# Performance work log

Measured on AMD Instinct MI355X. Metric: run time of the kernel, lower is better.

The kernel has to match this reference:

```python
import jax, jax.numpy as jnp
import numpy as np
from jax import lax

TOPK = 32
EPS = 1e-5


def setup_inputs() -> dict:
    key = jax.random.key(0)
    k1, k2, k3, k4 = jax.random.split(key, 4)
    t, b, dim = 1024, 2, 1024
    heads, num_keys, dim_head = 4, 512, 256
    dim_query = heads * dim_head  # 1024
    x = jax.random.normal(k1, (t, b, dim), dtype=jnp.float32)
    # nn.Linear default init ~ U(-1/sqrt(in), 1/sqrt(in)); scaled normal is fine as data
    Wq = jax.random.normal(k2, (dim, dim_query), dtype=jnp.float32) * (1.0 / np.sqrt(dim))
    gamma = jnp.ones((dim_query,), dtype=jnp.float32)
    beta = jnp.zeros((dim_query,), dtype=jnp.float32)
    # init_weights: keys std = 1/last_dim; values std = 1/sqrt(dim)
    keys = jax.random.normal(k3, (heads, num_keys, 2, dim_head // 2), dtype=jnp.float32) * (1.0 / (dim_head // 2))
    values = jax.random.normal(k4, (num_keys ** 2, dim), dtype=jnp.float32) * (1.0 / np.sqrt(dim))
    return {"x": x, "Wq": Wq, "gamma": gamma, "beta": beta, "keys": keys, "values": values}


def reference(x, Wq, gamma, beta, keys, values):
    t, b, e = x.shape
    h, n, _, dh2 = keys.shape  # heads, num_keys, 2, dim_head//2
    k = TOPK

    # queries = LayerNorm(x @ Wq)
    q = jnp.einsum('tbe,ef->tbf', x, Wq)  # (t, b, h*2*dh2)
    mu = jnp.mean(q, axis=-1, keepdims=True)
    var = jnp.var(q, axis=-1, keepdims=True)
    q = (q - mu) / jnp.sqrt(var + EPS) * gamma + beta

    # chunk into two halves of the query dim, each reshaped to (h, dh2)
    q = jnp.stack(jnp.split(q, 2, axis=-1)).reshape(2, t, b, h, dh2)  # (p=2, t, b, h, d)

    # scores against product keys
    dots = jnp.einsum('ptbhd,hnpd->tbhpn', q, keys)  # (t, b, h, 2, n)
    scores, indices = lax.top_k(dots, k)             # (t, b, h, 2, k)

    s1, s2 = scores[..., 0, :], scores[..., 1, :]
    i1, i2 = indices[..., 0, :], indices[..., 1, :]

    # cartesian product of the two top-k sets
    all_scores = (s1[..., :, None] + s2[..., None, :]).reshape(t, b, h, k * k)
    all_indices = (i1[..., :, None] * n + i2[..., None, :]).reshape(t, b, h, k * k)

    final_scores, final_idx = lax.top_k(all_scores, k)              # (t, b, h, k)
    value_indices = jnp.take_along_axis(all_indices, final_idx, axis=-1)
    attn = jax.nn.softmax(final_scores, axis=-1)

    value_indices = value_indices.reshape(t * b, h * k)
    attn = attn.reshape(t * b, h * k)

    # EmbeddingBag(mode='sum') with per_sample_weights
    gathered = values[value_indices]                 # (t*b, h*k, e)
    out = jnp.einsum('nk,nke->ne', attn, gathered)
    return out.reshape(t, b, e)
```

## Files before the change

### kernel.cpp

```cpp
#include <hip/hip_runtime.h>
#include <math.h>

#define NTOK 2048
#define DIM  1024
#define NHEAD 4
#define NKEY 512
#define DH   128
#define TK   32

typedef __attribute__((ext_vector_type(8))) short bf16x8;
typedef __attribute__((ext_vector_type(4))) float f32x4;

__device__ __forceinline__ unsigned short f2bf(float f) {
    unsigned int u = __float_as_uint(f);
    u += 0x7fff + ((u >> 16) & 1);
    return (unsigned short)(u >> 16);
}
__device__ __forceinline__ float bf2f(unsigned short h) {
    return __uint_as_float(((unsigned int)h) << 16);
}
__device__ __forceinline__ void split3(float f, unsigned short& h, unsigned short& m, unsigned short& l) {
    h = f2bf(f);
    float r1 = f - bf2f(h);
    m = f2bf(r1);
    l = f2bf(r1 - bf2f(m));
}
__device__ __forceinline__ void gll16(const void* g, void* l) {
    __builtin_amdgcn_global_load_lds((const __attribute__((address_space(1))) unsigned int*)g,
                                     (__attribute__((address_space(3))) unsigned int*)l, 16, 0, 0);
}

__global__ __launch_bounds__(256) void k_prep(const float* __restrict__ x,
                                              const float* __restrict__ Wq,
                                              const float* __restrict__ keys,
                                              unsigned short* __restrict__ X1,
                                              unsigned short* __restrict__ X2,
                                              unsigned short* __restrict__ X3,
                                              unsigned short* __restrict__ W1,
                                              unsigned short* __restrict__ W2,
                                              unsigned short* __restrict__ W3,
                                              unsigned short* __restrict__ K1,
                                              unsigned short* __restrict__ K2,
                                              unsigned short* __restrict__ K3) {
    __shared__ float f[64][33];
    const int b = blockIdx.x, tid = threadIdx.x;
    if (b < 2048) {
        int i = b * 256 + tid;
        float4 v = ((const float4*)x)[i];
        ushort4 hh, mm, ll;
        split3(v.x, hh.x, mm.x, ll.x); split3(v.y, hh.y, mm.y, ll.y);
        split3(v.z, hh.z, mm.z, ll.z); split3(v.w, hh.w, mm.w, ll.w);
        ((ushort4*)X1)[i] = hh; ((ushort4*)X2)[i] = mm; ((ushort4*)X3)[i] = ll;
    } else if (b < 2560) {
        const int ff = b - 2048;
        const int kt = (ff & 15) * 64, nt = (ff >> 4) * 32;
#pragma unroll
        for (int i = 0; i < 8; ++i) {
            int idx = tid + i * 256;
            int nl = idx & 31, kl = idx >> 5;
            f[kl][nl] = Wq[(size_t)(kt + kl) * DIM + nt + nl];
        }
        __syncthreads();
#pragma unroll
        for (int i = 0; i < 2; ++i) {
            int idx = tid + i * 256;
            int k4 = (idx & 15) * 4, nl = idx >> 4;
            ushort4 hh, mm, ll;
            split3(f[k4 + 0][nl], hh.x, mm.x, ll.x);
            split3(f[k4 + 1][nl], hh.y, mm.y, ll.y);
            split3(f[k4 + 2][nl], hh.z, mm.z, ll.z);
            split3(f[k4 + 3][nl], hh.w, mm.w, ll.w);
            *(ushort4*)(W1 + (size_t)(nt + nl) * DIM + kt + k4) = hh;
            *(ushort4*)(W2 + (size_t)(nt + nl) * DIM + kt + k4) = mm;
            *(ushort4*)(W3 + (size_t)(nt + nl) * DIM + kt + k4) = ll;
        }
    } else {
        int i = (b - 2560) * 256 + tid;
        float4 v = ((const float4*)keys)[i];
        ushort4 hh, mm, ll;
        split3(v.x, hh.x, mm.x, ll.x); split3(v.y, hh.y, mm.y, ll.y);
        split3(v.z, hh.z, mm.z, ll.z); split3(v.w, hh.w, mm.w, ll.w);
        ((ushort4*)K1)[i] = hh; ((ushort4*)K2)[i] = mm; ((ushort4*)K3)[i] = ll;
    }
}

__global__ __launch_bounds__(256) void k_gemm(const unsigned short* __restrict__ A1,
                                              const unsigned short* __restrict__ A2,
                                              const unsigned short* __restrict__ A3,
                                              const unsigned short* __restrict__ B1,
                                              const unsigned short* __restrict__ B2,
                                              const unsigned short* __restrict__ B3,
                                              float* __restrict__ C) {
    __shared__ alignas(16) unsigned short sA1[128 * 64];
    __shared__ alignas(16) unsigned short sA2[128 * 64];
    __shared__ alignas(16) unsigned short sA3[128 * 64];
    __shared__ alignas(16) unsigned short sB1[64 * 64];
    __shared__ alignas(16) unsigned short sB2[64 * 64];
    __shared__ alignas(16) unsigned short sB3[64 * 64];
    const int tid = threadIdx.x;
    const int lane = tid & 63, wid = tid >> 6;
    const int bm = blockIdx.x * 128, bn = blockIdx.y * 64;
    const int wr = (wid >> 1) * 64, wc = (wid & 1) * 32;
    f32x4 acc[4][2];
#pragma unroll
    for (int m = 0; m < 4; ++m)
#pragma unroll
        for (int n = 0; n < 2; ++n) acc[m][n] = (f32x4){0.f, 0.f, 0.f, 0.f};

    for (int kt = 0; kt < DIM; kt += 64) {
#pragma unroll
        for (int i = 0; i < 4; ++i) {
            int c = wid * 256 + i * 64 + lane;
            int row = c >> 3, kc = c & 7;
            int sk = (kc ^ (row & 7)) * 8;
            size_t ga = (size_t)(bm + row) * DIM + kt + sk;
            size_t lo = (size_t)(wid * 256 + i * 64) * 16;
            gll16(A1 + ga, (char*)sA1 + lo);
            gll16(A2 + ga, (char*)sA2 + lo);
            gll16(A3 + ga, (char*)sA3 + lo);
        }
#pragma unroll
        for (int i = 0; i < 2; ++i) {
            int c = wid * 128 + i * 64 + lane;
            int row = c >> 3, kc = c & 7;
            int sk = (kc ^ (row & 7)) * 8;
            size_t ga = (size_t)(bn + row) * DIM + kt + sk;
            size_t lo = (size_t)(wid * 128 + i * 64) * 16;
            gll16(B1 + ga, (char*)sB1 + lo);
            gll16(B2 + ga, (char*)sB2 + lo);
            gll16(B3 + ga, (char*)sB3 + lo);
        }
        __syncthreads();
#pragma unroll
        for (int ks = 0; ks < 2; ++ks) {
            bf16x8 a1[4], a2[4], a3[4], b1[2], b2[2], b3[2];
#pragma unroll
            for (int m = 0; m < 4; ++m) {
                int row = wr + m * 16 + (lane & 15);
                int ch = (ks * 4 + (lane >> 4)) ^ (row & 7);
                int off = row * 64 + ch * 8;
                a1[m] = *(const bf16x8*)(sA1 + off);
                a2[m] = *(const bf16x8*)(sA2 + off);
                a3[m] = *(const bf16x8*)(sA3 + off);
            }
#pragma unroll
            for (int n = 0; n < 2; ++n) {
                int row = wc + n * 16 + (lane & 15);
                int ch = (ks * 4 + (lane >> 4)) ^ (row & 7);
                int off = row * 64 + ch * 8;
                b1[n] = *(const bf16x8*)(sB1 + off);
                b2[n] = *(const bf16x8*)(sB2 + off);
                b3[n] = *(const bf16x8*)(sB3 + off);
            }
#pragma unroll
            for (int m = 0; m < 4; ++m)
#pragma unroll
                for (int n = 0; n < 2; ++n) {
                    acc[m][n] = __builtin_amdgcn_mfma_f32_16x16x32_bf16(a1[m], b1[n], acc[m][n], 0, 0, 0);
                    acc[m][n] = __builtin_amdgcn_mfma_f32_16x16x32_bf16(a1[m], b2[n], acc[m][n], 0, 0, 0);
                    acc[m][n] = __builtin_amdgcn_mfma_f32_16x16x32_bf16(a2[m], b1[n], acc[m][n], 0, 0, 0);
                    acc[m][n] = __builtin_amdgcn_mfma_f32_16x16x32_bf16(a2[m], b2[n], acc[m][n], 0, 0, 0);
                    acc[m][n] = __builtin_amdgcn_mfma_f32_16x16x32_bf16(a1[m], b3[n], acc[m][n], 0, 0, 0);
                    acc[m][n] = __builtin_amdgcn_mfma_f32_16x16x32_bf16(a3[m], b1[n], acc[m][n], 0, 0, 0);
                }
        }
        __syncthreads();
    }
#pragma unroll
    for (int m = 0; m < 4; ++m)
#pragma unroll
        for (int n = 0; n < 2; ++n)
#pragma unroll
            for (int j = 0; j < 4; ++j) {
                int row = bm + wr + m * 16 + (lane >> 4) * 4 + j;
                int col = bn + wc + n * 16 + (lane & 15);
                C[(size_t)row * DIM + col] = acc[m][n][j];
            }
}

__global__ __launch_bounds__(256) void k_ln(const float* __restrict__ Q,
                                            const float* __restrict__ gamma,
                                            const float* __restrict__ beta,
                                            unsigned short* __restrict__ q1,
                                            unsigned short* __restrict__ q2,
                                            unsigned short* __restrict__ q3) {
    const int row = blockIdx.x, tid = threadIdx.x;
    float4 v = *(const float4*)(Q + (size_t)row * DIM + tid * 4);
    float s  = v.x + v.y + v.z + v.w;
    float s2 = v.x * v.x + v.y * v.y + v.z * v.z + v.w * v.w;
#pragma unroll
    for (int off = 32; off > 0; off >>= 1) {
        s  += __shfl_down(s, off);
        s2 += __shfl_down(s2, off);
    }
    __shared__ float ps[4], ps2[4];
    const int wid = tid >> 6, lane = tid & 63;
    if (lane == 0) { ps[wid] = s; ps2[wid] = s2; }
    __syncthreads();
    s  = ps[0] + ps[1] + ps[2] + ps[3];
    s2 = ps2[0] + ps2[1] + ps2[2] + ps2[3];
    const float mu  = s * (1.0f / DIM);
    const float var = s2 * (1.0f / DIM) - mu * mu;
    const float inv = rsqrtf(var + 1e-5f);
    float4 g  = *(const float4*)(gamma + tid * 4);
    float4 be = *(const float4*)(beta + tid * 4);
    float o0 = (v.x - mu) * inv * g.x + be.x;
    float o1 = (v.y - mu) * inv * g.y + be.y;
    float o2 = (v.z - mu) * inv * g.z + be.z;
    float o3 = (v.w - mu) * inv * g.w + be.w;
    ushort4 hh, mm, ll;
    split3(o0, hh.x, mm.x, ll.x); split3(o1, hh.y, mm.y, ll.y);
    split3(o2, hh.z, mm.z, ll.z); split3(o3, hh.w, mm.w, ll.w);
    *(ushort4*)(q1 + (size_t)row * DIM + tid * 4) = hh;
    *(ushort4*)(q2 + (size_t)row * DIM + tid * 4) = mm;
    *(ushort4*)(q3 + (size_t)row * DIM + tid * 4) = ll;
}

__global__ __launch_bounds__(256) void k_dotsM(const unsigned short* __restrict__ Q1,
                                               const unsigned short* __restrict__ Q2,
                                               const unsigned short* __restrict__ Q3,
                                               const unsigned short* __restrict__ K1,
                                               const unsigned short* __restrict__ K2,
                                               const unsigned short* __restrict__ K3,
                                               float* __restrict__ D) {
    __shared__ alignas(16) unsigned short sA1[64 * 128];
    __shared__ alignas(16) unsigned short sA2[64 * 128];
    __shared__ alignas(16) unsigned short sA3[64 * 128];
    __shared__ alignas(16) unsigned short sB1[64 * 128];
    __shared__ alignas(16) unsigned short sB2[64 * 128];
    __shared__ alignas(16) unsigned short sB3[64 * 128];
    const int tid = threadIdx.x;
    const int lane = tid & 63, wid = tid >> 6;
    const int bm = blockIdx.x * 64, bn = blockIdx.y * 64;
    const int hp = blockIdx.z, h = hp >> 1, p = hp & 1;
    const int qoff = p * 512 + h * 128;
    const size_t kbase = (size_t)h * (NKEY * 2 * DH) + (size_t)p * DH;
#pragma unroll
    for (int i = 0; i < 4; ++i) {
        int c = wid * 256 + i * 64 + lane;
        int row = c >> 4, kc = c & 15;
        int sk = (kc ^ (row & 15)) * 8;
        size_t qa = (size_t)(bm + row) * DIM + qoff + sk;
        size_t ka = kbase + (size_t)(bn + row) * (2 * DH) + sk;
        size_t lo = (size_t)(wid * 256 + i * 64) * 16;
        gll16(Q1 + qa, (char*)sA1 + lo);
        gll16(Q2 + qa, (char*)sA2 + lo);
        gll16(Q3 + qa, (char*)sA3 + lo);
        gll16(K1 + ka, (char*)sB1 + lo);
        gll16(K2 + ka, (char*)sB2 + lo);
        gll16(K3 + ka, (char*)sB3 + lo);
    }
    __syncthreads();
    const int wr = (wid >> 1) * 32, wc = (wid & 1) * 32;
    f32x4 acc[2][2];
#pragma unroll
    for (int m = 0; m < 2; ++m)
#pragma unroll
        for (int n = 0; n < 2; ++n) acc[m][n] = (f32x4){0.f, 0.f, 0.f, 0.f};
#pragma unroll
    for (int ks = 0; ks < 4; ++ks) {
        bf16x8 a1[2], a2[2], a3[2], b1[2], b2[2], b3[2];
#pragma unroll
        for (int m = 0; m < 2; ++m) {
            int row = wr + m * 16 + (lane & 15);
            int ch = (ks * 4 + (lane >> 4)) ^ (row & 15);
            int off = row * 128 + ch * 8;
            a1[m] = *(const bf16x8*)(sA1 + off);
            a2[m] = *(const bf16x8*)(sA2 + off);
            a3[m] = *(const bf16x8*)(sA3 + off);
        }
#pragma unroll
        for (int n = 0; n < 2; ++n) {
            int row = wc + n * 16 + (lane & 15);
            int ch = (ks * 4 + (lane >> 4)) ^ (row & 15);
            int off = row * 128 + ch * 8;
            b1[n] = *(const bf16x8*)(sB1 + off);
            b2[n] = *(const bf16x8*)(sB2 + off);
            b3[n] = *(const bf16x8*)(sB3 + off);
        }
#pragma unroll
        for (int m = 0; m < 2; ++m)
#pragma unroll
            for (int n = 0; n < 2; ++n) {
                acc[m][n] = __builtin_amdgcn_mfma_f32_16x16x32_bf16(a1[m], b1[n], acc[m][n], 0, 0, 0);
                acc[m][n] = __builtin_amdgcn_mfma_f32_16x16x32_bf16(a1[m], b2[n], acc[m][n], 0, 0, 0);
                acc[m][n] = __builtin_amdgcn_mfma_f32_16x16x32_bf16(a2[m], b1[n], acc[m][n], 0, 0, 0);
                acc[m][n] = __builtin_amdgcn_mfma_f32_16x16x32_bf16(a2[m], b2[n], acc[m][n], 0, 0, 0);
                acc[m][n] = __builtin_amdgcn_mfma_f32_16x16x32_bf16(a1[m], b3[n], acc[m][n], 0, 0, 0);
                acc[m][n] = __builtin_amdgcn_mfma_f32_16x16x32_bf16(a3[m], b1[n], acc[m][n], 0, 0, 0);
            }
    }
#pragma unroll
    for (int m = 0; m < 2; ++m)
#pragma unroll
        for (int n = 0; n < 2; ++n)
#pragma unroll
            for (int j = 0; j < 4; ++j) {
                int row = bm + wr + m * 16 + (lane >> 4) * 4 + j;
                int col = bn + wc + n * 16 + (lane & 15);
                D[(size_t)row * 4096 + h * 1024 + p * 512 + col] = acc[m][n][j];
            }
}

template<int NV>
__device__ __forceinline__ bool bisect_tau(const float (&v)[NV], float& tau_out, int& c_out) {
    float lo = v[0], hi = v[0];
#pragma unroll
    for (int i = 1; i < NV; ++i) { lo = fminf(lo, v[i]); hi = fmaxf(hi, v[i]); }
#pragma unroll
    for (int off = 1; off < 64; off <<= 1) {
        lo = fminf(lo, __shfl_xor(lo, off));
        hi = fmaxf(hi, __shfl_xor(hi, off));
    }
    float tau = 0.5f * (lo + hi);
    for (int it = 0; it < 24; ++it) {
        int cl = 0;
#pragma unroll
        for (int i = 0; i < NV; ++i) cl += (v[i] >= tau) ? 1 : 0;
#pragma unroll
        for (int off = 1; off < 64; off <<= 1) cl += __shfl_xor(cl, off);
        if (cl >= 32 && cl <= 64) { tau_out = tau; c_out = cl; return true; }
        if (cl < 32) hi = tau; else lo = tau;
        float nt = 0.5f * (lo + hi);
        if (nt == tau || nt == lo || nt == hi) break;
        tau = nt;
    }
    return false;
}

__device__ __forceinline__ void bitonic64(float& sv, int& sn, int lane) {
#pragma unroll
    for (int k = 2; k <= 64; k <<= 1) {
#pragma unroll
        for (int j = k >> 1; j >= 1; j >>= 1) {
            float ov = __shfl_xor(sv, j);
            int   on = __shfl_xor(sn, j);
            bool lower   = (lane & j) == 0;
            bool descseg = (lane & k) == 0;
            bool keepwin = (lower == descseg);
            bool iwin = (sv > ov) || (sv == ov && sn < on);
            if (keepwin != iwin) { sv = ov; sn = on; }
        }
    }
}

__global__ __launch_bounds__(256) void k_topk_gather(const float* __restrict__ D,
                                                     const float* __restrict__ V,
                                                     float* __restrict__ out) {
    const int tid = threadIdx.x;
    const int wid = tid >> 6, lane = tid & 63;
    const int token = blockIdx.x;
    const int h = wid;
    __shared__ float s1[NHEAD][TK], s2[NHEAD][TK], wv[NHEAD][TK];
    __shared__ int   i1[NHEAD][TK], i2[NHEAD][TK], cc[NHEAD][TK];
    __shared__ float candV[NHEAD][64];
    __shared__ int   candN[NHEAD][64];
    __shared__ float wgt[128];
    __shared__ int   gidx[128];

    const size_t base = (size_t)token * 4096 + (size_t)h * 1024;
    float v1[8], v2[8];
#pragma unroll
    for (int i = 0; i < 8; ++i) {
        v1[i] = D[base + lane + (i << 6)];
        v2[i] = D[base + 512 + lane + (i << 6)];
    }

#pragma unroll
    for (int half = 0; half < 2; ++half) {
        float (&vv)[8] = half ? v2 : v1;
        float* sO = half ? &s2[h][0] : &s1[h][0];
        int*   iO = half ? &i2[h][0] : &i1[h][0];
        float tau; int c;
        if (bisect_tau<8>(vv, tau, c)) {
            int cum = 0;
#pragma unroll
            for (int i = 0; i < 8; ++i) {
                bool f = (vv[i] >= tau);
                unsigned long long bal = __ballot(f);
                int slot = cum + __popcll(bal & ((1ull << lane) - 1ull));
                if (f) { candV[h][slot] = vv[i]; candN[h][slot] = lane + (i << 6); }
                cum += __popcll(bal);
            }
            asm volatile("s_waitcnt lgkmcnt(0)" ::: "memory");
            float sv = (lane < c) ? candV[h][lane] : -INFINITY;
            int   sn = (lane < c) ? candN[h][lane] : 0x7FFFFFFF;
            bitonic64(sv, sn, lane);
            if (lane < TK) { sO[lane] = sv; iO[lane] = sn; }
        } else {
            for (int it = 0; it < TK; ++it) {
                float bv = vv[0]; int bi = 0;
#pragma unroll
                for (int i = 1; i < 8; ++i) if (vv[i] > bv) { bv = vv[i]; bi = i; }
                int bn = lane + (bi << 6);
#pragma unroll
                for (int off = 1; off < 64; off <<= 1) {
                    float ov = __shfl_xor(bv, off);
                    int   on = __shfl_xor(bn, off);
                    if (ov > bv || (ov == bv && on < bn)) { bv = ov; bn = on; }
                }
#pragma unroll
                for (int i = 0; i < 8; ++i)
                    if (bn == lane + (i << 6)) vv[i] = -INFINITY;
                if (lane == 0) { sO[it] = bv; iO[it] = bn; }
            }
        }
    }

    float cv[16];
#pragma unroll
    for (int s = 0; s < 16; ++s) {
        int c = lane + (s << 6);
        cv[s] = s1[h][c >> 5] + s2[h][c & 31];
    }
    {
        float tau; int c;
        if (bisect_tau<16>(cv, tau, c)) {
            int cum = 0;
#pragma unroll
            for (int s = 0; s < 16; ++s) {
                bool f = (cv[s] >= tau);
                unsigned long long bal = __ballot(f);
                int slot = cum + __popcll(bal & ((1ull << lane) - 1ull));
                if (f) { candV[h][slot] = cv[s]; candN[h][slot] = lane + (s << 6); }
                cum += __popcll(bal);
            }
            asm volatile("s_waitcnt lgkmcnt(0)" ::: "memory");
            float sv = (lane < c) ? candV[h][lane] : -INFINITY;
            int   sn = (lane < c) ? candN[h][lane] : 0x7FFFFFFF;
            bitonic64(sv, sn, lane);
            float m = __shfl(sv, 0);
            float w = (lane < TK) ? expf(sv - m) : 0.0f;
            float sum = w;
#pragma unroll
            for (int off = 1; off < 64; off <<= 1) sum += __shfl_xor(sum, off);
            if (lane < TK) {
                wgt[h * TK + lane]  = w / sum;
                gidx[h * TK + lane] = i1[h][sn >> 5] * NKEY + i2[h][sn & 31];
            }
        } else {
            float m = 0.f, sum = 0.f;
            for (int it = 0; it < TK; ++it) {
                float bv = cv[0]; int bs = 0;
#pragma unroll
                for (int s = 1; s < 16; ++s) if (cv[s] > bv) { bv = cv[s]; bs = s; }
                int bc = lane + (bs << 6);
#pragma unroll
                for (int off = 1; off < 64; off <<= 1) {
                    float ov = __shfl_xor(bv, off);
                    int   oc = __shfl_xor(bc, off);
                    if (ov > bv || (ov == bv && oc < bc)) { bv = ov; bc = oc; }
                }
#pragma unroll
                for (int s = 0; s < 16; ++s)
                    if (bc == lane + (s << 6)) cv[s] = -INFINITY;
                if (it == 0) m = bv;
                float w = expf(bv - m);
                sum += w;
                if (lane == 0) { wv[h][it] = w; cc[h][it] = bc; }
            }
            if (lane < TK) {
                int c2 = cc[h][lane];
                wgt[h * TK + lane]  = wv[h][lane] / sum;
                gidx[h * TK + lane] = i1[h][c2 >> 5] * NKEY + i2[h][c2 & 31];
            }
        }
    }
    __syncthreads();

    const int col = tid * 4;
    float4 acc = make_float4(0.f, 0.f, 0.f, 0.f);
#pragma unroll 8
    for (int j = 0; j < 128; ++j) {
        const float4 v = *(const float4*)(V + (size_t)gidx[j] * DIM + col);
        const float wj = wgt[j];
        acc.x = fmaf(wj, v.x, acc.x);
        acc.y = fmaf(wj, v.y, acc.y);
        acc.z = fmaf(wj, v.z, acc.z);
        acc.w = fmaf(wj, v.w, acc.w);
    }
    *(float4*)(out + (size_t)token * DIM + col) = acc;
}

extern "C" void kernel_launch(void* const* d_in, const int* in_sizes, int n_in,
                              void* d_out, int out_size, void* d_ws, size_t ws_size,
                              hipStream_t stream) {
    const float* x      = (const float*)d_in[0];
    const float* Wq     = (const float*)d_in[1];
    const float* gamma  = (const float*)d_in[2];
    const float* beta   = (const float*)d_in[3];
    const float* keys   = (const float*)d_in[4];
    const float* values = (const float*)d_in[5];

    char* w = (char*)d_ws;
    float* D = (float*)w;
    float* q = D;
    unsigned short* X1 = (unsigned short*)(w + ((size_t)34 << 20));
    unsigned short* X2 = (unsigned short*)(w + ((size_t)38 << 20));
    unsigned short* X3 = (unsigned short*)(w + ((size_t)42 << 20));
    unsigned short* W1 = (unsigned short*)(w + ((size_t)46 << 20));
    unsigned short* W2 = (unsigned short*)(w + ((size_t)48 << 20));
    unsigned short* W3 = (unsigned short*)(w + ((size_t)50 << 20));
    unsigned short* q1 = (unsigned short*)(w + ((size_t)52 << 20));
    unsigned short* q2 = (unsigned short*)(w + ((size_t)56 << 20));
    unsigned short* q3 = (unsigned short*)(w + ((size_t)60 << 20));
    unsigned short* K1 = (unsigned short*)(w + ((size_t)64 << 20));
    unsigned short* K2 = (unsigned short*)(w + ((size_t)65 << 20));
    unsigned short* K3 = (unsigned short*)(w + ((size_t)66 << 20));

    k_prep<<<3072, 256, 0, stream>>>(x, Wq, keys, X1, X2, X3, W1, W2, W3, K1, K2, K3);
    k_gemm<<<dim3(16, 16), 256, 0, stream>>>(X1, X2, X3, W1, W2, W3, q);
    k_ln<<<NTOK, 256, 0, stream>>>(q, gamma, beta, q1, q2, q3);
    k_dotsM<<<dim3(32, 8, 8), 256, 0, stream>>>(q1, q2, q3, K1, K2, K3, D);
    k_topk_gather<<<NTOK, 256, 0, stream>>>(D, values, (float*)d_out);
}
```

Before: 257.9 us.

## Fuse bf16 triple-splitting of x and LayerNorm output into GEMM tile loads

```diff
diff --git a/kernel.cpp b/kernel.cpp
--- a/kernel.cpp
+++ b/kernel.cpp
@@ -29,13 +29,17 @@
     __builtin_amdgcn_global_load_lds((const __attribute__((address_space(1))) unsigned int*)g,
                                      (__attribute__((address_space(3))) unsigned int*)l, 16, 0, 0);
 }
-
-__global__ __launch_bounds__(256) void k_prep(const float* __restrict__ x,
-                                              const float* __restrict__ Wq,
+__device__ __forceinline__ void split8(const float (&vv)[8], bf16x8& h8, bf16x8& m8, bf16x8& l8) {
+#pragma unroll
+    for (int j = 0; j < 8; ++j) {
+        unsigned short h, m, l;
+        split3(vv[j], h, m, l);
+        h8[j] = (short)h; m8[j] = (short)m; l8[j] = (short)l;
+    }
+}
+
+__global__ __launch_bounds__(256) void k_prep(const float* __restrict__ Wq,
                                               const float* __restrict__ keys,
-                                              unsigned short* __restrict__ X1,
-                                              unsigned short* __restrict__ X2,
-                                              unsigned short* __restrict__ X3,
                                               unsigned short* __restrict__ W1,
                                               unsigned short* __restrict__ W2,
                                               unsigned short* __restrict__ W3,
@@ -44,16 +48,8 @@
                                               unsigned short* __restrict__ K3) {
     __shared__ float f[64][33];
     const int b = blockIdx.x, tid = threadIdx.x;
-    if (b < 2048) {
-        int i = b * 256 + tid;
-        float4 v = ((const float4*)x)[i];
-        ushort4 hh, mm, ll;
-        split3(v.x, hh.x, mm.x, ll.x); split3(v.y, hh.y, mm.y, ll.y);
-        split3(v.z, hh.z, mm.z, ll.z); split3(v.w, hh.w, mm.w, ll.w);
-        ((ushort4*)X1)[i] = hh; ((ushort4*)X2)[i] = mm; ((ushort4*)X3)[i] = ll;
-    } else if (b < 2560) {
-        const int ff = b - 2048;
-        const int kt = (ff & 15) * 64, nt = (ff >> 4) * 32;
+    if (b < 512) {
+        const int kt = (b & 15) * 64, nt = (b >> 4) * 32;
 #pragma unroll
         for (int i = 0; i < 8; ++i) {
             int idx = tid + i * 256;
@@ -75,7 +71,7 @@
             *(ushort4*)(W3 + (size_t)(nt + nl) * DIM + kt + k4) = ll;
         }
     } else {
-        int i = (b - 2560) * 256 + tid;
+        int i = (b - 512) * 256 + tid;
         float4 v = ((const float4*)keys)[i];
         ushort4 hh, mm, ll;
         split3(v.x, hh.x, mm.x, ll.x); split3(v.y, hh.y, mm.y, ll.y);
@@ -84,9 +80,7 @@
     }
 }
 
-__global__ __launch_bounds__(256) void k_gemm(const unsigned short* __restrict__ A1,
-                                              const unsigned short* __restrict__ A2,
-                                              const unsigned short* __restrict__ A3,
+__global__ __launch_bounds__(256) void k_gemm(const float* __restrict__ X,
                                               const unsigned short* __restrict__ B1,
                                               const unsigned short* __restrict__ B2,
                                               const unsigned short* __restrict__ B3,
@@ -109,17 +103,6 @@
 
     for (int kt = 0; kt < DIM; kt += 64) {
 #pragma unroll
-        for (int i = 0; i < 4; ++i) {
-            int c = wid * 256 + i * 64 + lane;
-            int row = c >> 3, kc = c & 7;
-            int sk = (kc ^ (row & 7)) * 8;
-            size_t ga = (size_t)(bm + row) * DIM + kt + sk;
-            size_t lo = (size_t)(wid * 256 + i * 64) * 16;
-            gll16(A1 + ga, (char*)sA1 + lo);
-            gll16(A2 + ga, (char*)sA2 + lo);
-            gll16(A3 + ga, (char*)sA3 + lo);
-        }
-#pragma unroll
         for (int i = 0; i < 2; ++i) {
             int c = wid * 128 + i * 64 + lane;
             int row = c >> 3, kc = c & 7;
@@ -130,6 +113,20 @@
             gll16(B2 + ga, (char*)sB2 + lo);
             gll16(B3 + ga, (char*)sB3 + lo);
         }
+#pragma unroll
+        for (int i = 0; i < 4; ++i) {
+            int c = wid * 256 + i * 64 + lane;
+            int row = c >> 3, kc8 = c & 7;
+            const float4* src = (const float4*)(X + (size_t)(bm + row) * DIM + kt + kc8 * 8);
+            float4 u0 = src[0], u1 = src[1];
+            float vv[8] = {u0.x, u0.y, u0.z, u0.w, u1.x, u1.y, u1.z, u1.w};
+            bf16x8 h8, m8, l8;
+            split8(vv, h8, m8, l8);
+            int dst = row * 64 + (kc8 ^ (row & 7)) * 8;
+            *(bf16x8*)(sA1 + dst) = h8;
+            *(bf16x8*)(sA2 + dst) = m8;
+            *(bf16x8*)(sA3 + dst) = l8;
+        }
         __syncthreads();
 #pragma unroll
         for (int ks = 0; ks < 2; ++ks) {
@@ -178,12 +175,8 @@
             }
 }
 
-__global__ __launch_bounds__(256) void k_ln(const float* __restrict__ Q,
-                                            const float* __restrict__ gamma,
-                                            const float* __restrict__ beta,
-                                            unsigned short* __restrict__ q1,
-                                            unsigned short* __restrict__ q2,
-                                            unsigned short* __restrict__ q3) {
+__global__ __launch_bounds__(256) void k_stats(const float* __restrict__ Q,
+                                               float2* __restrict__ stats) {
     const int row = blockIdx.x, tid = threadIdx.x;
     float4 v = *(const float4*)(Q + (size_t)row * DIM + tid * 4);
     float s  = v.x + v.y + v.z + v.w;
@@ -197,28 +190,19 @@
     const int wid = tid >> 6, lane = tid & 63;
     if (lane == 0) { ps[wid] = s; ps2[wid] = s2; }
     __syncthreads();
-    s  = ps[0] + ps[1] + ps[2] + ps[3];
-    s2 = ps2[0] + ps2[1] + ps2[2] + ps2[3];
-    const float mu  = s * (1.0f / DIM);
-    const float var = s2 * (1.0f / DIM) - mu * mu;
-    const float inv = rsqrtf(var + 1e-5f);
-    float4 g  = *(const float4*)(gamma + tid * 4);
-    float4 be = *(const float4*)(beta + tid * 4);
-    float o0 = (v.x - mu) * inv * g.x + be.x;
-    float o1 = (v.y - mu) * inv * g.y + be.y;
-    float o2 = (v.z - mu) * inv * g.z + be.z;
-    float o3 = (v.w - mu) * inv * g.w + be.w;
-    ushort4 hh, mm, ll;
-    split3(o0, hh.x, mm.x, ll.x); split3(o1, hh.y, mm.y, ll.y);
-    split3(o2, hh.z, mm.z, ll.z); split3(o3, hh.w, mm.w, ll.w);
-    *(ushort4*)(q1 + (size_t)row * DIM + tid * 4) = hh;
-    *(ushort4*)(q2 + (size_t)row * DIM + tid * 4) = mm;
-    *(ushort4*)(q3 + (size_t)row * DIM + tid * 4) = ll;
-}
-
-__global__ __launch_bounds__(256) void k_dotsM(const unsigned short* __restrict__ Q1,
-                                               const unsigned short* __restrict__ Q2,
-                                               const unsigned short* __restrict__ Q3,
+    if (tid == 0) {
+        s  = ps[0] + ps[1] + ps[2] + ps[3];
+        s2 = ps2[0] + ps2[1] + ps2[2] + ps2[3];
+        const float mu  = s * (1.0f / DIM);
+        const float var = s2 * (1.0f / DIM) - mu * mu;
+        stats[row] = make_float2(mu, rsqrtf(var + 1e-5f));
+    }
+}
+
+__global__ __launch_bounds__(256) void k_dotsF(const float* __restrict__ Q,
+                                               const float2* __restrict__ stats,
+                                               const float* __restrict__ gamma,
+                                               const float* __restrict__ beta,
                                                const unsigned short* __restrict__ K1,
                                                const unsigned short* __restrict__ K2,
                                                const unsigned short* __restrict__ K3,
@@ -238,17 +222,31 @@
 #pragma unroll
     for (int i = 0; i < 4; ++i) {
         int c = wid * 256 + i * 64 + lane;
-        int row = c >> 4, kc = c & 15;
-        int sk = (kc ^ (row & 15)) * 8;
-        size_t qa = (size_t)(bm + row) * DIM + qoff + sk;
+        int row = c >> 4, kc8 = c & 15;
+        int sk = (kc8 ^ (row & 15)) * 8;
         size_t ka = kbase + (size_t)(bn + row) * (2 * DH) + sk;
         size_t lo = (size_t)(wid * 256 + i * 64) * 16;
-        gll16(Q1 + qa, (char*)sA1 + lo);
-        gll16(Q2 + qa, (char*)sA2 + lo);
-        gll16(Q3 + qa, (char*)sA3 + lo);
         gll16(K1 + ka, (char*)sB1 + lo);
         gll16(K2 + ka, (char*)sB2 + lo);
         gll16(K3 + ka, (char*)sB3 + lo);
+        float2 st = stats[bm + row];
+        int colbase = qoff + kc8 * 8;
+        const float4* qs = (const float4*)(Q + (size_t)(bm + row) * DIM + colbase);
+        float4 u0 = qs[0], u1 = qs[1];
+        const float4* g4 = (const float4*)(gamma + colbase);
+        const float4* b4 = (const float4*)(beta + colbase);
+        float4 g0 = g4[0], g1 = g4[1], e0 = b4[0], e1 = b4[1];
+        float vv[8] = {
+            (u0.x - st.x) * st.y * g0.x + e0.x, (u0.y - st.x) * st.y * g0.y + e0.y,
+            (u0.z - st.x) * st.y * g0.z + e0.z, (u0.w - st.x) * st.y * g0.w + e0.w,
+            (u1.x - st.x) * st.y * g1.x + e1.x, (u1.y - st.x) * st.y * g1.y + e1.y,
+            (u1.z - st.x) * st.y * g1.z + e1.z, (u1.w - st.x) * st.y * g1.w + e1.w };
+        bf16x8 h8, m8, l8;
+        split8(vv, h8, m8, l8);
+        int dst = row * 128 + (kc8 ^ (row & 15)) * 8;
+        *(bf16x8*)(sA1 + dst) = h8;
+        *(bf16x8*)(sA2 + dst) = m8;
+        *(bf16x8*)(sA3 + dst) = l8;
     }
     __syncthreads();
     const int wr = (wid >> 1) * 32, wc = (wid & 1) * 32;
@@ -494,23 +492,18 @@
 
     char* w = (char*)d_ws;
     float* D = (float*)w;
-    float* q = D;
-    unsigned short* X1 = (unsigned short*)(w + ((size_t)34 << 20));
-    unsigned short* X2 = (unsigned short*)(w + ((size_t)38 << 20));
-    unsigned short* X3 = (unsigned short*)(w + ((size_t)42 << 20));
+    float* q = (float*)(w + ((size_t)32 << 20));
     unsigned short* W1 = (unsigned short*)(w + ((size_t)46 << 20));
     unsigned short* W2 = (unsigned short*)(w + ((size_t)48 << 20));
     unsigned short* W3 = (unsigned short*)(w + ((size_t)50 << 20));
-    unsigned short* q1 = (unsigned short*)(w + ((size_t)52 << 20));
-    unsigned short* q2 = (unsigned short*)(w + ((size_t)56 << 20));
-    unsigned short* q3 = (unsigned short*)(w + ((size_t)60 << 20));
+    float2*         st = (float2*)        (w + ((size_t)52 << 20));
     unsigned short* K1 = (unsigned short*)(w + ((size_t)64 << 20));
     unsigned short* K2 = (unsigned short*)(w + ((size_t)65 << 20));
     unsigned short* K3 = (unsigned short*)(w + ((size_t)66 << 20));
 
-    k_prep<<<3072, 256, 0, stream>>>(x, Wq, keys, X1, X2, X3, W1, W2, W3, K1, K2, K3);
-    k_gemm<<<dim3(16, 16), 256, 0, stream>>>(X1, X2, X3, W1, W2, W3, q);
-    k_ln<<<NTOK, 256, 0, stream>>>(q, gamma, beta, q1, q2, q3);
-    k_dotsM<<<dim3(32, 8, 8), 256, 0, stream>>>(q1, q2, q3, K1, K2, K3, D);
+    k_prep<<<1024, 256, 0, stream>>>(Wq, keys, W1, W2, W3, K1, K2, K3);
+    k_gemm<<<dim3(16, 16), 256, 0, stream>>>(x, W1, W2, W3, q);
+    k_stats<<<NTOK, 256, 0, stream>>>(q, st);
+    k_dotsF<<<dim3(32, 8, 8), 256, 0, stream>>>(q, st, gamma, beta, K1, K2, K3, D);
     k_topk_gather<<<NTOK, 256, 0, stream>>>(D, values, (float*)d_out);
 }
```

After: 277.5 us. 1.08x slower.
